# Optimization experiments

Hardware: AMD Instinct MI355X
Metric: run time of the kernel (lower is better)

## Reference

```python
import jax, jax.numpy as jnp
import numpy as np

N = 2048      # number of nodes
D = 128       # node_dim
QK = 64       # qk_dim == value_dim (code reshapes v with qk_dim)
H = 8         # n_heads
E = 8         # edge_dim


def _l2norm(x):
    return x / (jnp.linalg.norm(x, axis=-1, keepdims=True) + 1e-8)


def setup_inputs() -> dict:
    key = jax.random.key(0)
    ks = jax.random.split(key, 10)
    nodes = jax.random.normal(ks[0], (N, D), jnp.float32)
    adj = (jax.random.uniform(ks[1], (N, N, 1)) < 0.1).astype(jnp.float32)
    adj = jnp.maximum(adj, jnp.eye(N, dtype=jnp.float32)[:, :, None])
    edges = jax.random.normal(ks[2], (N, N, E), jnp.float32)
    # Linear weights stored as (out_features, in_features), eqx convention
    WQ = jax.random.normal(ks[3], (QK * H, D), jnp.float32) / np.sqrt(D)
    WK = jax.random.normal(ks[4], (QK * H, D), jnp.float32) / np.sqrt(D)
    WV = jax.random.normal(ks[5], (QK * H, D), jnp.float32) / np.sqrt(D)
    Wo = jax.random.normal(ks[6], (D, QK * H), jnp.float32) / np.sqrt(QK * H)
    bo = jax.random.normal(ks[7], (D,), jnp.float32) * 0.01
    We = jax.random.normal(ks[8], (H, E), jnp.float32) / np.sqrt(E)
    Weo = jax.random.normal(ks[9], (E, H), jnp.float32) / np.sqrt(H)
    return dict(nodes=nodes, adj=adj, edges=edges, WQ=WQ, WK=WK, WV=WV,
                Wo=Wo, bo=bo, We=We, Weo=Weo)


def reference(nodes, adj, edges, WQ, WK, WV, Wo, bo, We, Weo):
    n = nodes.shape[0]
    # per-node projections; reshape(N, qk_dim, n_heads): head is fastest axis
    q = (nodes @ WQ.T).reshape(n, QK, H)
    k = (nodes @ WK.T).reshape(n, QK, H)
    v = (nodes @ WV.T).reshape(n, QK, H)

    scores = jnp.einsum('ndh,Ndh->nNh', q, k) / jnp.sqrt(jnp.float32(QK))

    # edge-feature modulation of attention scores
    we = jnp.einsum('nNe,he->nNh', edges, We) * adj          # [N,N,H]
    scores = scores * we

    # edge update: residual + out-projection, then L2 normalize
    edges_out = _l2norm(edges + jnp.einsum('nNh,eh->nNe', scores, Weo))

    # masked softmax over axis=1 with initial=min(scores*adj) (jnn.softmax semantics)
    mask = adj > 0                                            # [N,N,1] -> broadcast
    init = jnp.min(scores * adj)
    neg = jnp.finfo(scores.dtype).min
    x_max = jnp.maximum(jnp.max(jnp.where(mask, scores, neg), axis=1, keepdims=True), init)
    x_max = jax.lax.stop_gradient(x_max)
    unnorm = jnp.where(mask, jnp.exp(scores - x_max), 0.0)
    attn = unnorm / jnp.sum(unnorm, axis=1, keepdims=True)    # [N,N,H]

    h = jnp.einsum('nNh,Ndh->ndh', attn, v).reshape(n, -1)    # [N, QK*H]
    nodes_out = _l2norm(nodes + h @ Wo.T + bo)
    return nodes_out, edges_out
```

## Files before the change

### kernel.cpp

```cpp
#include <hip/hip_runtime.h>
#include <hip/hip_bf16.h>

#define N_NODES 2048
#define D_NODE 128
#define QK_DIM 64
#define N_HEADS 8
#define E_DIM 8
#define EXP_SHIFT 24.0f

typedef __hip_bfloat16 bf16;
typedef unsigned short u16;
typedef __attribute__((ext_vector_type(8))) short bf16x8v;
typedef __attribute__((ext_vector_type(4))) float f32x4v;

__device__ __forceinline__ float bf2f(bf16 x) { return __bfloat162float(x); }
__device__ __forceinline__ float u2f(u16 u) { return __uint_as_float(((unsigned)u) << 16); }
__device__ __forceinline__ u16 f2bf(float f) {
  unsigned u = __float_as_uint(f);
  unsigned r = u + 0x7FFFu + ((u >> 16) & 1u);
  return (u16)(r >> 16);
}

__device__ __forceinline__ void unpack2(unsigned u, float& a, float& b) {
  union { unsigned x; float f; } lo, hi;
  lo.x = u << 16; hi.x = u & 0xffff0000u;
  a = lo.f; b = hi.f;
}
__device__ __forceinline__ void unpack8(uint4 u, float* f) {
  unpack2(u.x, f[0], f[1]); unpack2(u.y, f[2], f[3]);
  unpack2(u.z, f[4], f[5]); unpack2(u.w, f[6], f[7]);
}

template <bool BF16>
__device__ __forceinline__ float ldv(const void* p, size_t i) {
  if constexpr (BF16) return bf2f(((const bf16*)p)[i]);
  else return ((const float*)p)[i];
}
template <bool BF16>
__device__ __forceinline__ void ld8v(const void* p, size_t i8, float* f) {
  if constexpr (BF16) {
    uint4 u = ((const uint4*)p)[i8];
    unpack8(u, f);
  } else {
    const float4* fp = (const float4*)p;
    float4 a = fp[2 * i8], b = fp[2 * i8 + 1];
    f[0] = a.x; f[1] = a.y; f[2] = a.z; f[3] = a.w;
    f[4] = b.x; f[5] = b.y; f[6] = b.z; f[7] = b.w;
  }
}
template <bool BF16>
__device__ __forceinline__ void stv(void* p, size_t i, float v) {
  if constexpr (BF16) ((bf16*)p)[i] = __float2bfloat16(v);
  else ((float*)p)[i] = v;
}
template <bool BF16>
__device__ __forceinline__ void st8v(void* p, size_t i8, const float* f) {
  if constexpr (BF16) {
    union { uint4 u; u16 b[8]; } ou;
#pragma unroll
    for (int e = 0; e < 8; e++) ou.b[e] = f2bf(f[e]);
    ((uint4*)p)[i8] = ou.u;
  } else {
    ((float4*)p)[2 * i8] = make_float4(f[0], f[1], f[2], f[3]);
    ((float4*)p)[2 * i8 + 1] = make_float4(f[4], f[5], f[6], f[7]);
  }
}

template <bool BF16>
__device__ __forceinline__ bf16x8v ld_frag(const void* p, size_t elem) {
  if constexpr (BF16) {
    return *(const bf16x8v*)((const u16*)p + elem);
  } else {
    const float4* fp = (const float4*)p;
    float4 a = fp[elem / 4], b = fp[elem / 4 + 1];
    union { bf16x8v v; u16 s[8]; } o;
    o.s[0] = f2bf(a.x); o.s[1] = f2bf(a.y); o.s[2] = f2bf(a.z); o.s[3] = f2bf(a.w);
    o.s[4] = f2bf(b.x); o.s[5] = f2bf(b.y); o.s[6] = f2bf(b.z); o.s[7] = f2bf(b.w);
    return o.v;
  }
}

__global__ void k_detect(const unsigned* __restrict__ adj_words, int* __restrict__ flag) {
  if (threadIdx.x == 0 && blockIdx.x == 0) {
    int b = 0;
    for (int i = 0; i < 64; i++)
      if ((adj_words[i] & 0xFFFFu) == 0x3F80u) b = 1;
    *flag = b;
  }
}

template <bool BF16>
__global__ __launch_bounds__(256) void k_proj(
    const int* __restrict__ flag,
    const void* __restrict__ nodes, const void* __restrict__ WQ,
    const void* __restrict__ WK, const void* __restrict__ WV,
    const void* __restrict__ Wo, float* __restrict__ WoT,
    u16* __restrict__ qhi, u16* __restrict__ qlo,
    u16* __restrict__ khi, u16* __restrict__ klo, u16* __restrict__ vT) {
  if ((*flag != 0) != BF16) return;
  int t = threadIdx.x;
  int g = blockIdx.y;
  if (g == 24) {
    int idx = ((int)blockIdx.x * 256 + t) * 2;
    int o = idx >> 9, f = idx & 511;
    WoT[(size_t)f * D_NODE + o] = ldv<BF16>(Wo, (size_t)o * 512 + f);
    WoT[(size_t)(f + 1) * D_NODE + o] = ldv<BF16>(Wo, (size_t)o * 512 + f + 1);
    return;
  }
  int n0 = blockIdx.x * 16;
  int mat = g >> 3;
  int h = g & 7;
  const void* W = (mat == 0) ? WQ : (mat == 1) ? WK : WV;
  int wv = t >> 6, lane = t & 63, m0 = lane & 15, quad = lane >> 4;
  int d = wv * 16 + m0;
  int wrow = d * 8 + h;
  f32x4v acc = {0.f, 0.f, 0.f, 0.f};
#pragma unroll
  for (int kk = 0; kk < 4; kk++) {
    bf16x8v af = ld_frag<BF16>(nodes, (size_t)(n0 + m0) * D_NODE + kk * 32 + quad * 8);
    bf16x8v bfr = ld_frag<BF16>(W, (size_t)wrow * D_NODE + kk * 32 + quad * 8);
    acc = __builtin_amdgcn_mfma_f32_16x16x32_bf16(af, bfr, acc, 0, 0, 0);
  }
  if (mat == 2) {
    union { unsigned w[2]; u16 s[4]; } ob;
#pragma unroll
    for (int reg = 0; reg < 4; reg++) ob.s[reg] = f2bf(acc[reg]);
    int n = n0 + quad * 4;
    unsigned* dst = (unsigned*)(vT + ((size_t)(h * QK_DIM + d)) * N_NODES + n);
    dst[0] = ob.w[0]; dst[1] = ob.w[1];
  } else {
    u16* hiP = (mat == 0) ? qhi : khi;
    u16* loP = (mat == 0) ? qlo : klo;
    float scale = (mat == 0) ? 0.125f : 1.f;
#pragma unroll
    for (int reg = 0; reg < 4; reg++) {
      int n = n0 + quad * 4 + reg;
      float vq = acc[reg] * scale;
      u16 hi = f2bf(vq);
      u16 lo = f2bf(vq - u2f(hi));
      size_t o = ((size_t)(h * N_NODES + n) << 6) + d;
      hiP[o] = hi; loP[o] = lo;
    }
  }
}

template <bool BF16>
__global__ __launch_bounds__(256, 2) void k_fused(
    const int* __restrict__ flag, int S,
    const void* __restrict__ adj, const void* __restrict__ edges,
    const void* __restrict__ We, const void* __restrict__ Weo,
    const u16* __restrict__ qhi, const u16* __restrict__ qlo,
    const u16* __restrict__ khi, const u16* __restrict__ klo,
    const u16* __restrict__ vT,
    float* __restrict__ hout_p, float* __restrict__ psum_p,
    void* __restrict__ out_base) {
  if ((*flag != 0) != BF16) return;
  __shared__ float We_s[N_HEADS][E_DIM];
  __shared__ float Weo_s[E_DIM][N_HEADS];
  __shared__ float wes[N_HEADS][16][33];
  __shared__ u16 p_tile[N_HEADS][16][32];
  int t = threadIdx.x;
  if (t < 64) { We_s[t >> 3][t & 7] = ldv<BF16>(We, t); Weo_s[t >> 3][t & 7] = ldv<BF16>(Weo, t); }
  int split = blockIdx.x, rt = blockIdx.y;
  int row0 = rt * 16;
  int nst = (N_NODES / 32) / S;
  int colbase = split * nst * 32;
  int r = t >> 4, cc = t & 15;
  int wv = t >> 6, lane = t & 63, m0 = lane & 15, quad = lane >> 4;
  float psum[N_HEADS];
#pragma unroll
  for (int h = 0; h < 8; h++) psum[h] = 0.f;
  f32x4v acc_pv[2][4];
#pragma unroll
  for (int hh = 0; hh < 2; hh++)
#pragma unroll
    for (int dc = 0; dc < 4; dc++) acc_pv[hh][dc] = (f32x4v){0.f, 0.f, 0.f, 0.f};

  void* edges_out = (char*)out_base + (size_t)N_NODES * D_NODE * (BF16 ? 2 : 4);

  int nrow = row0 + r;
  float a_c0, a_c1;
  float e8_c[16];
  {
    size_t p0 = (size_t)nrow * N_NODES + colbase + cc;
    a_c0 = ldv<BF16>(adj, p0);
    a_c1 = ldv<BF16>(adj, p0 + 16);
    ld8v<BF16>(edges, p0, e8_c);
    ld8v<BF16>(edges, p0 + 16, e8_c + 8);
  }

  for (int ct = 0; ct < nst; ct++) {
    int col0 = colbase + ct * 32;
    size_t pair0 = (size_t)nrow * N_NODES + col0 + cc;
    int ctn = (ct + 1 < nst) ? (ct + 1) : 0;
    size_t pn = (size_t)nrow * N_NODES + colbase + ctn * 32 + cc;
    float a_n0 = ldv<BF16>(adj, pn);
    float a_n1 = ldv<BF16>(adj, pn + 16);
    float e8_n[16];
    ld8v<BF16>(edges, pn, e8_n);
    ld8v<BF16>(edges, pn + 16, e8_n + 8);

    __syncthreads();
#pragma unroll
    for (int h = 0; h < 8; h++) {
      float w0 = 0.f, w1 = 0.f;
#pragma unroll
      for (int e = 0; e < 8; e++) {
        w0 += e8_c[e] * We_s[h][e];
        w1 += e8_c[e + 8] * We_s[h][e];
      }
      wes[h][r][cc] = w0 * a_c0;
      wes[h][r][cc + 16] = w1 * a_c1;
    }
    __syncthreads();
#pragma unroll
    for (int hh = 0; hh < 2; hh++) {
      int h = wv * 2 + hh;
      size_t qbase = ((size_t)(h * N_NODES + row0 + m0) << 6) + quad * 8;
      bf16x8v qh0 = *(const bf16x8v*)(qhi + qbase);
      bf16x8v ql0 = *(const bf16x8v*)(qlo + qbase);
      bf16x8v qh1 = *(const bf16x8v*)(qhi + qbase + 32);
      bf16x8v ql1 = *(const bf16x8v*)(qlo + qbase + 32);
#pragma unroll
      for (int ch = 0; ch < 2; ch++) {
        int c0 = col0 + ch * 16;
        size_t kbase = ((size_t)(h * N_NODES + c0 + m0) << 6) + quad * 8;
        bf16x8v kh0 = *(const bf16x8v*)(khi + kbase);
        bf16x8v kl0 = *(const bf16x8v*)(klo + kbase);
        bf16x8v kh1 = *(const bf16x8v*)(khi + kbase + 32);
        bf16x8v kl1 = *(const bf16x8v*)(klo + kbase + 32);
        f32x4v acc = {0.f, 0.f, 0.f, 0.f};
        acc = __builtin_amdgcn_mfma_f32_16x16x32_bf16(qh0, kh0, acc, 0, 0, 0);
        acc = __builtin_amdgcn_mfma_f32_16x16x32_bf16(qh0, kl0, acc, 0, 0, 0);
        acc = __builtin_amdgcn_mfma_f32_16x16x32_bf16(ql0, kh0, acc, 0, 0, 0);
        acc = __builtin_amdgcn_mfma_f32_16x16x32_bf16(qh1, kh1, acc, 0, 0, 0);
        acc = __builtin_amdgcn_mfma_f32_16x16x32_bf16(qh1, kl1, acc, 0, 0, 0);
        acc = __builtin_amdgcn_mfma_f32_16x16x32_bf16(ql1, kh1, acc, 0, 0, 0);
#pragma unroll
        for (int reg = 0; reg < 4; reg++) {
          int i = quad * 4 + reg;
          wes[h][i][ch * 16 + m0] *= acc[reg];
        }
      }
    }
    __syncthreads();
#pragma unroll
    for (int half = 0; half < 2; half++) {
      float sm[8];
#pragma unroll
      for (int h = 0; h < 8; h++) sm[h] = wes[h][r][half * 16 + cc];
      float av = half ? a_c1 : a_c0;
      float ss = 0.f, eo[8];
#pragma unroll
      for (int e = 0; e < 8; e++) {
        float x = e8_c[half * 8 + e];
#pragma unroll
        for (int h = 0; h < 8; h++) x += sm[h] * Weo_s[e][h];
        eo[e] = x; ss += x * x;
      }
      float inv = 1.f / (sqrtf(ss) + 1e-8f);
#pragma unroll
      for (int e = 0; e < 8; e++) eo[e] *= inv;
      st8v<BF16>(edges_out, pair0 + half * 16, eo);
#pragma unroll
      for (int h = 0; h < 8; h++) {
        float p = (av != 0.f) ? __expf(sm[h] - EXP_SHIFT) : 0.f;
        psum[h] += p;
        p_tile[h][r][half * 16 + cc] = f2bf(p);
      }
    }
    __syncthreads();
#pragma unroll
    for (int hh = 0; hh < 2; hh++) {
      int h = wv * 2 + hh;
      bf16x8v ap = *(const bf16x8v*)(&p_tile[h][0][0] + m0 * 32 + quad * 8);
#pragma unroll
      for (int dc = 0; dc < 4; dc++) {
        bf16x8v bp = *(const bf16x8v*)(vT + ((size_t)(h * QK_DIM + dc * 16 + m0)) * N_NODES + col0 + quad * 8);
        acc_pv[hh][dc] = __builtin_amdgcn_mfma_f32_16x16x32_bf16(ap, bp, acc_pv[hh][dc], 0, 0, 0);
      }
    }
    a_c0 = a_n0; a_c1 = a_n1;
#pragma unroll
    for (int e = 0; e < 16; e++) e8_c[e] = e8_n[e];
  }
#pragma unroll
  for (int h = 0; h < 8; h++) {
    float x = psum[h];
    x += __shfl_xor(x, 1); x += __shfl_xor(x, 2);
    x += __shfl_xor(x, 4); x += __shfl_xor(x, 8);
    if ((t & 15) == 0)
      psum_p[((size_t)(row0 + r)) * (S * 8) + split * 8 + h] = x;
  }
#pragma unroll
  for (int hh = 0; hh < 2; hh++) {
    int h = wv * 2 + hh;
#pragma unroll
    for (int dc = 0; dc < 4; dc++) {
#pragma unroll
      for (int reg = 0; reg < 4; reg++) {
        int nn = row0 + quad * 4 + reg;
        hout_p[((size_t)nn * S + split) * 512 + h * 64 + dc * 16 + m0] = acc_pv[hh][dc][reg];
      }
    }
  }
}

template <bool BF16>
__global__ __launch_bounds__(128) void k_out(
    const int* __restrict__ flag, int S,
    const void* __restrict__ nodes, const float* __restrict__ WoT,
    const void* __restrict__ bo,
    const float* __restrict__ hout_p, const float* __restrict__ psum_p,
    void* __restrict__ out_base) {
  if ((*flag != 0) != BF16) return;
  int n = blockIdx.x, t = threadIdx.x;
  __shared__ float hv[QK_DIM * N_HEADS];
  __shared__ float inv_s[N_HEADS];
  __shared__ float red[128];
  if (t < 64) red[t] = (t < S * 8) ? psum_p[(size_t)n * (S * 8) + t] : 0.f;
  __syncthreads();
  if (t < 8) {
    float tot = 0.f;
#pragma unroll
    for (int s = 0; s < 8; s++) tot += red[s * 8 + t];
    inv_s[t] = (tot > 0.f) ? 1.f / tot : 0.f;
  }
  __syncthreads();
  for (int i = t; i < QK_DIM * N_HEADS; i += 128) {
    int d = i >> 3, hh = i & 7;
    float acc = 0.f;
    for (int s = 0; s < S; s++)
      acc += hout_p[((size_t)n * S + s) * 512 + hh * 64 + d];
    hv[i] = acc * inv_s[hh];
  }
  __syncthreads();
  float val = ldv<BF16>(nodes, (size_t)n * D_NODE + t) + ldv<BF16>(bo, t);
#pragma unroll 8
  for (int j = 0; j < 512; j++) val += WoT[(size_t)j * D_NODE + t] * hv[j];
  red[t] = val * val;
  __syncthreads();
  for (int s = 64; s > 0; s >>= 1) {
    if (t < s) red[t] += red[t + s];
    __syncthreads();
  }
  float ss = red[0];
  stv<BF16>(out_base, (size_t)n * D_NODE + t, val / (sqrtf(ss) + 1e-8f));
}

extern "C" void kernel_launch(void* const* d_in, const int* in_sizes, int n_in,
                              void* d_out, int out_size, void* d_ws, size_t ws_size,
                              hipStream_t stream) {
  const void* nodes = d_in[0];
  const void* adj   = d_in[1];
  const void* edges = d_in[2];
  const void* WQ = d_in[3];
  const void* WK = d_in[4];
  const void* WV = d_in[5];
  const void* Wo = d_in[6];
  const void* bo = d_in[7];
  const void* We = d_in[8];
  const void* Weo = d_in[9];

  char* w = (char*)d_ws;
  int* flag = (int*)w;
  size_t off = 256;
  const size_t PLANE = (size_t)N_HEADS * N_NODES * QK_DIM * 2;
  u16* qhi = (u16*)(w + off);  off += PLANE;
  u16* qlo = (u16*)(w + off);  off += PLANE;
  u16* khi = (u16*)(w + off);  off += PLANE;
  u16* klo = (u16*)(w + off);  off += PLANE;
  u16* vT  = (u16*)(w + off);  off += PLANE;
  float* WoT = (float*)(w + off);  off += (size_t)512 * D_NODE * 4;

  int S = 8;
  while (S > 1 && off + (size_t)S * ((size_t)N_NODES * 512 * 4 + N_NODES * 8 * 4) > ws_size)
    S >>= 1;
  float* hout_p = (float*)(w + off);
  off += (size_t)S * N_NODES * 512 * 4;
  float* psum_p = (float*)(w + off);

  k_detect<<<1, 64, 0, stream>>>((const unsigned*)adj, flag);

  dim3 g1(N_NODES / 16, 25);
  k_proj<false><<<g1, 256, 0, stream>>>(flag, nodes, WQ, WK, WV, Wo, WoT, qhi, qlo, khi, klo, vT);
  k_proj<true ><<<g1, 256, 0, stream>>>(flag, nodes, WQ, WK, WV, Wo, WoT, qhi, qlo, khi, klo, vT);

  dim3 g2(S, N_NODES / 16);
  k_fused<false><<<g2, 256, 0, stream>>>(flag, S, adj, edges, We, Weo,
                                         qhi, qlo, khi, klo, vT, hout_p, psum_p, d_out);
  k_fused<true ><<<g2, 256, 0, stream>>>(flag, S, adj, edges, We, Weo,
                                         qhi, qlo, khi, klo, vT, hout_p, psum_p, d_out);

  k_out<false><<<N_NODES, 128, 0, stream>>>(flag, S, nodes, WoT, bo, hout_p, psum_p, d_out);
  k_out<true ><<<N_NODES, 128, 0, stream>>>(flag, S, nodes, WoT, bo, hout_p, psum_p, d_out);
}
```

Measured before the change: 410.9 us.

## Defer PV MFMA by one tile and fold edge-weight calc into epilogue

Drops the separate edge-weight pass and its barrier. The QK MFMA results now go into a transposed shared tile as vector stores, and the per-head edge weights are computed inline in the edge-update phase. The P*V MFMA for the previous column tile is shifted into the same phase as the current tile's QK MFMAs, with one trailing P*V after the loop, so each iteration needs two barriers instead of four. This adds some per-thread recomputation of the We dot products and keeps p_tile live across iterations, relying on the barrier ordering to keep it correct.

New measurement: 458.0 us. 1.11x slower.

```diff
diff --git a/kernel.cpp b/kernel.cpp
--- a/kernel.cpp
+++ b/kernel.cpp
@@ -157,7 +157,7 @@
   if ((*flag != 0) != BF16) return;
   __shared__ float We_s[N_HEADS][E_DIM];
   __shared__ float Weo_s[E_DIM][N_HEADS];
-  __shared__ float wes[N_HEADS][16][33];
+  __shared__ float smod_t[N_HEADS][32][20];
   __shared__ u16 p_tile[N_HEADS][16][32];
   int t = threadIdx.x;
   if (t < 64) { We_s[t >> 3][t & 7] = ldv<BF16>(We, t); Weo_s[t >> 3][t & 7] = ldv<BF16>(Weo, t); }
@@ -201,18 +201,7 @@
     ld8v<BF16>(edges, pn + 16, e8_n + 8);
 
     __syncthreads();
-#pragma unroll
-    for (int h = 0; h < 8; h++) {
-      float w0 = 0.f, w1 = 0.f;
-#pragma unroll
-      for (int e = 0; e < 8; e++) {
-        w0 += e8_c[e] * We_s[h][e];
-        w1 += e8_c[e + 8] * We_s[h][e];
-      }
-      wes[h][r][cc] = w0 * a_c0;
-      wes[h][r][cc + 16] = w1 * a_c1;
-    }
-    __syncthreads();
+
 #pragma unroll
     for (int hh = 0; hh < 2; hh++) {
       int h = wv * 2 + hh;
@@ -236,24 +225,40 @@
         acc = __builtin_amdgcn_mfma_f32_16x16x32_bf16(qh1, kh1, acc, 0, 0, 0);
         acc = __builtin_amdgcn_mfma_f32_16x16x32_bf16(qh1, kl1, acc, 0, 0, 0);
         acc = __builtin_amdgcn_mfma_f32_16x16x32_bf16(ql1, kh1, acc, 0, 0, 0);
-#pragma unroll
-        for (int reg = 0; reg < 4; reg++) {
-          int i = quad * 4 + reg;
-          wes[h][i][ch * 16 + m0] *= acc[reg];
+        *(f32x4v*)&smod_t[h][ch * 16 + m0][quad * 4] = acc;
+      }
+    }
+    if (ct) {
+      int colk = col0 - 32;
+#pragma unroll
+      for (int hh = 0; hh < 2; hh++) {
+        int h = wv * 2 + hh;
+        bf16x8v ap = *(const bf16x8v*)(&p_tile[h][0][0] + m0 * 32 + quad * 8);
+#pragma unroll
+        for (int dc = 0; dc < 4; dc++) {
+          bf16x8v bp = *(const bf16x8v*)(vT + ((size_t)(h * QK_DIM + dc * 16 + m0)) * N_NODES + colk + quad * 8);
+          acc_pv[hh][dc] = __builtin_amdgcn_mfma_f32_16x16x32_bf16(ap, bp, acc_pv[hh][dc], 0, 0, 0);
         }
       }
     }
     __syncthreads();
+
 #pragma unroll
     for (int half = 0; half < 2; half++) {
+      float av = half ? a_c1 : a_c0;
+      const float* e8h = e8_c + half * 8;
       float sm[8];
 #pragma unroll
-      for (int h = 0; h < 8; h++) sm[h] = wes[h][r][half * 16 + cc];
-      float av = half ? a_c1 : a_c0;
+      for (int h = 0; h < 8; h++) {
+        float we = 0.f;
+#pragma unroll
+        for (int e = 0; e < 8; e++) we += e8h[e] * We_s[h][e];
+        sm[h] = smod_t[h][half * 16 + cc][r] * (we * av);
+      }
       float ss = 0.f, eo[8];
 #pragma unroll
       for (int e = 0; e < 8; e++) {
-        float x = e8_c[half * 8 + e];
+        float x = e8h[e];
 #pragma unroll
         for (int h = 0; h < 8; h++) x += sm[h] * Weo_s[e][h];
         eo[e] = x; ss += x * x;
@@ -269,20 +274,24 @@
         p_tile[h][r][half * 16 + cc] = f2bf(p);
       }
     }
-    __syncthreads();
+    a_c0 = a_n0; a_c1 = a_n1;
+#pragma unroll
+    for (int e = 0; e < 16; e++) e8_c[e] = e8_n[e];
+  }
+
+  __syncthreads();
+  {
+    int colk = colbase + (nst - 1) * 32;
 #pragma unroll
     for (int hh = 0; hh < 2; hh++) {
       int h = wv * 2 + hh;
       bf16x8v ap = *(const bf16x8v*)(&p_tile[h][0][0] + m0 * 32 + quad * 8);
 #pragma unroll
       for (int dc = 0; dc < 4; dc++) {
-        bf16x8v bp = *(const bf16x8v*)(vT + ((size_t)(h * QK_DIM + dc * 16 + m0)) * N_NODES + col0 + quad * 8);
+        bf16x8v bp = *(const bf16x8v*)(vT + ((size_t)(h * QK_DIM + dc * 16 + m0)) * N_NODES + colk + quad * 8);
         acc_pv[hh][dc] = __builtin_amdgcn_mfma_f32_16x16x32_bf16(ap, bp, acc_pv[hh][dc], 0, 0, 0);
       }
     }
-    a_c0 = a_n0; a_c1 = a_n1;
-#pragma unroll
-    for (int e = 0; e < 16; e++) e8_c[e] = e8_n[e];
   }
 #pragma unroll
   for (int h = 0; h < 8; h++) {
```

## Batch eight nodes per block in output projection with shared Wo tiles

Applied to the files above, without the earlier changes.

The output-projection kernel now handles 8 nodes per 256-thread block instead of one node per 128-thread block. Wo^T is staged through shared memory in 64-row chunks and reused across 4 nodes per thread, cutting the repeated global reads of the 256 KB weight matrix. The L2-norm reduction now uses wave shuffles instead of a shared-memory tree. This needs about 52 KB of shared memory and launches only 256 blocks, which may limit occupancy on a large GPU.

Measured after the change: 434.2 us. +5.7%, slower.

```diff
diff --git a/kernel.cpp b/kernel.cpp
--- a/kernel.cpp
+++ b/kernel.cpp
@@ -307,45 +307,74 @@
 }
 
 template <bool BF16>
-__global__ __launch_bounds__(128) void k_out(
+__global__ __launch_bounds__(256, 2) void k_out(
     const int* __restrict__ flag, int S,
     const void* __restrict__ nodes, const float* __restrict__ WoT,
     const void* __restrict__ bo,
     const float* __restrict__ hout_p, const float* __restrict__ psum_p,
     void* __restrict__ out_base) {
   if ((*flag != 0) != BF16) return;
-  int n = blockIdx.x, t = threadIdx.x;
-  __shared__ float hv[QK_DIM * N_HEADS];
-  __shared__ float inv_s[N_HEADS];
-  __shared__ float red[128];
-  if (t < 64) red[t] = (t < S * 8) ? psum_p[(size_t)n * (S * 8) + t] : 0.f;
+  int t = threadIdx.x;
+  int n0 = blockIdx.x * 8;
+  __shared__ float hv_s[8][512];
+  __shared__ float inv_s[8][8];
+  __shared__ float wchunk[64][128];
+  __shared__ float part_s[4][4];
+  if (t < 64) {
+    int node = t >> 3, h = t & 7;
+    float tot = 0.f;
+    for (int s = 0; s < S; s++) tot += psum_p[(size_t)(n0 + node) * (S * 8) + s * 8 + h];
+    inv_s[node][h] = (tot > 0.f) ? 1.f / tot : 0.f;
+  }
   __syncthreads();
-  if (t < 8) {
-    float tot = 0.f;
-#pragma unroll
-    for (int s = 0; s < 8; s++) tot += red[s * 8 + t];
-    inv_s[t] = (tot > 0.f) ? 1.f / tot : 0.f;
-  }
-  __syncthreads();
-  for (int i = t; i < QK_DIM * N_HEADS; i += 128) {
-    int d = i >> 3, hh = i & 7;
+  for (int i = t; i < 8 * 512; i += 256) {
+    int node = i >> 9, f = i & 511;
+    int d = f >> 3, hh = f & 7;
     float acc = 0.f;
     for (int s = 0; s < S; s++)
-      acc += hout_p[((size_t)n * S + s) * 512 + hh * 64 + d];
-    hv[i] = acc * inv_s[hh];
+      acc += hout_p[((size_t)(n0 + node) * S + s) * 512 + hh * 64 + d];
+    hv_s[node][f] = acc * inv_s[node][hh];
+  }
+  int o = t & 127, half = t >> 7;
+  float acc[4] = {0.f, 0.f, 0.f, 0.f};
+  for (int j0 = 0; j0 < 512; j0 += 64) {
+    __syncthreads();
+    const float4* src = (const float4*)(WoT + (size_t)j0 * 128);
+    float4* dst = (float4*)&wchunk[0][0];
+    for (int i = t; i < 64 * 128 / 4; i += 256) dst[i] = src[i];
+    __syncthreads();
+#pragma unroll
+    for (int jj = 0; jj < 64; jj++) {
+      float w = wchunk[jj][o];
+#pragma unroll
+      for (int k = 0; k < 4; k++)
+        acc[k] += w * hv_s[half * 4 + k][j0 + jj];
+    }
+  }
+  float val[4], s2[4];
+#pragma unroll
+  for (int k = 0; k < 4; k++) {
+    int n = n0 + half * 4 + k;
+    val[k] = ldv<BF16>(nodes, (size_t)n * D_NODE + o) + ldv<BF16>(bo, o) + acc[k];
+    s2[k] = val[k] * val[k];
+  }
+#pragma unroll
+  for (int off = 1; off < 64; off <<= 1) {
+#pragma unroll
+    for (int k = 0; k < 4; k++) s2[k] += __shfl_xor(s2[k], off);
+  }
+  int wave = t >> 6;
+  if ((t & 63) == 0) {
+#pragma unroll
+    for (int k = 0; k < 4; k++) part_s[wave][k] = s2[k];
   }
   __syncthreads();
-  float val = ldv<BF16>(nodes, (size_t)n * D_NODE + t) + ldv<BF16>(bo, t);
-#pragma unroll 8
-  for (int j = 0; j < 512; j++) val += WoT[(size_t)j * D_NODE + t] * hv[j];
-  red[t] = val * val;
-  __syncthreads();
-  for (int s = 64; s > 0; s >>= 1) {
-    if (t < s) red[t] += red[t + s];
-    __syncthreads();
-  }
-  float ss = red[0];
-  stv<BF16>(out_base, (size_t)n * D_NODE + t, val / (sqrtf(ss) + 1e-8f));
+#pragma unroll
+  for (int k = 0; k < 4; k++) {
+    float ss = part_s[half * 2][k] + part_s[half * 2 + 1][k];
+    int n = n0 + half * 4 + k;
+    stv<BF16>(out_base, (size_t)n * D_NODE + o, val[k] / (sqrtf(ss) + 1e-8f));
+  }
 }
 
 extern "C" void kernel_launch(void* const* d_in, const int* in_sizes, int n_in,
@@ -392,6 +421,6 @@
   k_fused<true ><<<g2, 256, 0, stream>>>(flag, S, adj, edges, We, Weo,
                                          qhi, qlo, khi, klo, vT, hout_p, psum_p, d_out);
 
-  k_out<false><<<N_NODES, 128, 0, stream>>>(flag, S, nodes, WoT, bo, hout_p, psum_p, d_out);
-  k_out<true ><<<N_NODES, 128, 0, stream>>>(flag, S, nodes, WoT, bo, hout_p, psum_p, d_out);
-}
+  k_out<false><<<N_NODES / 8, 256, 0, stream>>>(flag, S, nodes, WoT, bo, hout_p, psum_p, d_out);
+  k_out<true ><<<N_NODES / 8, 256, 0, stream>>>(flag, S, nodes, WoT, bo, hout_p, psum_p, d_out);
+}
```
